# Performance work log

Hardware: AMD Instinct MI355X
Metric: run time of the kernel (lower is better)

## Reference

```python
import jax, jax.numpy as jnp
import numpy as np

N = 100000
E = 1600000
D_IN = 50
D_H = 128
D_OUT = 128
EPS = 1e-5


def setup_inputs() -> dict:
    key = jax.random.key(0)
    ks = jax.random.split(key, 24)
    def w(k, shape, fan_in):
        return jax.random.normal(k, shape, jnp.float32) / np.sqrt(fan_in)
    inp = {
        'x': jax.random.normal(ks[0], (N, D_IN), jnp.float32),
        'edge_src': jax.random.randint(ks[1], (E,), 0, N, jnp.int32),
        'edge_dst': jax.random.randint(ks[2], (E,), 0, N, jnp.int32),
        # SAGEConv 1: D_IN -> D_H
        'Wl1': w(ks[3], (D_IN, D_H), D_IN), 'Wr1': w(ks[4], (D_IN, D_H), D_IN), 'b1': jnp.zeros((D_H,), jnp.float32),
        # SAGEConv 2: D_H -> D_H
        'Wl2': w(ks[5], (D_H, D_H), D_H), 'Wr2': w(ks[6], (D_H, D_H), D_H), 'b2': jnp.zeros((D_H,), jnp.float32),
        # SAGEConv 3: D_H -> D_OUT
        'Wl3': w(ks[7], (D_H, D_OUT), D_H), 'Wr3': w(ks[8], (D_H, D_OUT), D_H), 'b3': jnp.zeros((D_OUT,), jnp.float32),
        # skip linears (no bias)
        'Ws1': w(ks[9], (D_IN, D_H), D_IN), 'Ws2': w(ks[10], (D_IN, D_H), D_IN),
        # LayerNorm affine
        'lnw1': jnp.ones((D_H,), jnp.float32), 'lnb1': jnp.zeros((D_H,), jnp.float32),
        'lnw2': jnp.ones((D_H,), jnp.float32), 'lnb2': jnp.zeros((D_H,), jnp.float32),
        'lnw3': jnp.ones((D_OUT,), jnp.float32), 'lnb3': jnp.zeros((D_OUT,), jnp.float32),
        # PReLU scalar slopes (PyG init 0.25)
        'a1': jnp.float32(0.25), 'a2': jnp.float32(0.25), 'a3': jnp.float32(0.25),
    }
    return inp


def _sage(x, src, dst, Wl, Wr, b):
    # mean aggregation of source features at destinations, then linear + root
    msg = x[src]                                              # [E, d]
    agg = jax.ops.segment_sum(msg, dst, num_segments=N)       # [N, d]
    cnt = jax.ops.segment_sum(jnp.ones((src.shape[0],), x.dtype), dst, num_segments=N)
    mean = agg / jnp.maximum(cnt, 1.0)[:, None]
    return mean @ Wl + x @ Wr + b


def _graph_ln(x, w, b):
    # PyG LayerNorm mode='graph', batch=None: normalize over all nodes+channels
    xc = x - jnp.mean(x)
    std = jnp.sqrt(jnp.mean(xc * xc))
    return (xc / (std + EPS)) * w + b


def _prelu(x, a):
    return jnp.where(x >= 0, x, a * x)


def reference(x, edge_src, edge_dst, Wl1, Wr1, b1, Wl2, Wr2, b2, Wl3, Wr3, b3,
              Ws1, Ws2, lnw1, lnb1, lnw2, lnb2, lnw3, lnb3, a1, a2, a3):
    h1 = _sage(x, edge_src, edge_dst, Wl1, Wr1, b1)
    h1 = _prelu(_graph_ln(h1, lnw1, lnb1), a1)
    h2 = _sage(h1 + x @ Ws1, edge_src, edge_dst, Wl2, Wr2, b2)
    h2 = _prelu(_graph_ln(h2, lnw2, lnb2), a2)
    ret = _sage(h1 + h2 + x @ Ws2, edge_src, edge_dst, Wl3, Wr3, b3)
    ret = _prelu(_graph_ln(ret, lnw3, lnb3), a3)
    return ret
```

## Files before the change

kernel.cpp:

```cpp
#include <hip/hip_runtime.h>

#define D_IN 50
#define LN_EPS 1e-5f
#define BSH 8
#define MAXB 512

typedef __bf16 bf16_t;
typedef bf16_t bf16x8 __attribute__((ext_vector_type(8)));
typedef bf16_t bf16x4 __attribute__((ext_vector_type(4)));
typedef float f32x4_t __attribute__((ext_vector_type(4)));
typedef float f32x2_t __attribute__((ext_vector_type(2)));

#define ACCP(r, A)                                                            \
    {                                                                         \
        A[0] += (f32x2_t){__uint_as_float((r).x << 16),                       \
                          __uint_as_float((r).x & 0xffff0000u)};              \
        A[1] += (f32x2_t){__uint_as_float((r).y << 16),                       \
                          __uint_as_float((r).y & 0xffff0000u)};              \
        A[2] += (f32x2_t){__uint_as_float((r).z << 16),                       \
                          __uint_as_float((r).z & 0xffff0000u)};              \
        A[3] += (f32x2_t){__uint_as_float((r).w << 16),                       \
                          __uint_as_float((r).w & 0xffff0000u)};              \
    }

__global__ void bucket_hist_k(const int* __restrict__ dst, int* __restrict__ bcnt,
                              double* __restrict__ lnacc, int e, int nb) {
    __shared__ int lh[MAXB];
    int t = threadIdx.x;
    if (blockIdx.x == 0 && t < 6) lnacc[t] = 0.0;
    for (int i = t; i < nb; i += 256) lh[i] = 0;
    __syncthreads();
    for (int i = blockIdx.x * 256 + t; i < e; i += gridDim.x * 256)
        atomicAdd(&lh[dst[i] >> BSH], 1);
    __syncthreads();
    for (int i = t; i < nb; i += 256) {
        int c = lh[i];
        if (c) atomicAdd(&bcnt[i * 16], c);
    }
}

__global__ void bscan_k(const int* __restrict__ bcnt, int* __restrict__ boff,
                        int* __restrict__ bpos, int nb, int e) {
    __shared__ int l[MAXB];
    int t = threadIdx.x;
    l[t] = (t < nb) ? bcnt[t * 16] : 0;
    __syncthreads();
    for (int off = 1; off < MAXB; off <<= 1) {
        int v = (t >= off) ? l[t - off] : 0;
        __syncthreads();
        l[t] += v;
        __syncthreads();
    }
    int excl = (t > 0) ? l[t - 1] : 0;
    if (t < nb) { boff[t] = excl; bpos[t * 16] = excl; }
    if (t == 0) boff[nb] = e;
}

__global__ void scatter_k(const int* __restrict__ src, const int* __restrict__ dst,
                          int* __restrict__ bpos, unsigned* __restrict__ pool,
                          int e, int nb) {
    __shared__ int lh[MAXB];
    __shared__ int lcur[MAXB];
    int t = threadIdx.x;
    for (int i = t; i < nb; i += 256) lh[i] = 0;
    __syncthreads();
    int chunk = (e + gridDim.x - 1) / gridDim.x;
    int s = blockIdx.x * chunk;
    int en = min(e, s + chunk);
    for (int i = s + t; i < en; i += 256)
        atomicAdd(&lh[dst[i] >> BSH], 1);
    __syncthreads();
    for (int i = t; i < nb; i += 256) {
        int c = lh[i];
        lcur[i] = c ? atomicAdd(&bpos[i * 16], c) : 0;
    }
    __syncthreads();
    for (int i = s + t; i < en; i += 256) {
        int d = dst[i];
        int p = atomicAdd(&lcur[d >> BSH], 1);
        pool[p] = (unsigned)src[i] | ((unsigned)(d & 255) << 17);
    }
}

__global__ void nhist_cfill_k(const unsigned* __restrict__ pool, const int* __restrict__ boff,
                              int* __restrict__ rp, int* __restrict__ col, int n) {
    __shared__ int lc[256];
    __shared__ int ls[256];
    __shared__ int lpos[256];
    int b = blockIdx.x, t = threadIdx.x;
    lc[t] = 0;
    __syncthreads();
    int s = boff[b], e = boff[b + 1];
    for (int i = s + t; i < e; i += 256) atomicAdd(&lc[pool[i] >> 17], 1);
    __syncthreads();
    int v = lc[t];
    ls[t] = v;
    __syncthreads();
    for (int off = 1; off < 256; off <<= 1) {
        int x = (t >= off) ? ls[t - off] : 0;
        __syncthreads();
        ls[t] += x;
        __syncthreads();
    }
    int excl = ls[t] - v;
    int nd = (b << BSH) + t;
    if (nd < n) rp[nd] = s + excl;
    if (nd == n - 1) rp[n] = e;
    lpos[t] = s + excl;
    __syncthreads();
    for (int i = s + t; i < e; i += 256) {
        unsigned pk = pool[i];
        int slot = atomicAdd(&lpos[pk >> 17], 1);
        col[slot] = (int)(pk & 0x1FFFFu);
    }
}

struct ConvDesc { const float* w; bf16_t* o; int kin; int kpad; };
struct ConvArgs { ConvDesc d[8]; };

__global__ void conv_w_k(ConvArgs args) {
    ConvDesc d = args.d[blockIdx.y];
    int i = blockIdx.x * 256 + threadIdx.x;
    int tot = 128 * d.kpad;
    if (i >= tot) return;
    int n = i / d.kpad, k = i - n * d.kpad;
    float v = (k < d.kin) ? d.w[(size_t)k * 128 + n] : 0.f;
    d.o[i] = (bf16_t)v;
}

__global__ void conv_x_k(const float* __restrict__ x, bf16_t* __restrict__ xb, int n) {
    int i = blockIdx.x * 256 + threadIdx.x;
    if (i >= n * 64) return;
    int node = i >> 6, k = i & 63;
    xb[i] = (k < D_IN) ? (bf16_t)x[node * D_IN + k] : (bf16_t)0.f;
}

__global__ void agg_bf64_k(const bf16_t* __restrict__ feat, const int* __restrict__ rp,
                           const int* __restrict__ col, bf16_t* __restrict__ mean, int n) {
    int wid = (blockIdx.x * blockDim.x + threadIdx.x) >> 6;
    int lane = threadIdx.x & 63;
    if (wid >= n) return;
    int start = rp[wid], end = rp[wid + 1];
    int lc = lane & 7;
    int g = lane >> 3;
    f32x2_t accA[4], accB[4];
#pragma unroll
    for (int k = 0; k < 4; k++) { accA[k] = (f32x2_t){0.f, 0.f}; accB[k] = (f32x2_t){0.f, 0.f}; }
    int e = start + g;
    if (e + 8 < end) {
        int i0 = col[e], i1 = col[e + 8];
        for (; e + 24 < end; e += 16) {
            uint4 r0 = *(const uint4*)(feat + (size_t)i0 * 64 + lc * 8);
            uint4 r1 = *(const uint4*)(feat + (size_t)i1 * 64 + lc * 8);
            i0 = col[e + 16];
            i1 = col[e + 24];
            ACCP(r0, accA);
            ACCP(r1, accB);
        }
        uint4 r0 = *(const uint4*)(feat + (size_t)i0 * 64 + lc * 8);
        uint4 r1 = *(const uint4*)(feat + (size_t)i1 * 64 + lc * 8);
        ACCP(r0, accA);
        ACCP(r1, accB);
        e += 16;
    }
    for (; e < end; e += 8) {
        uint4 r0 = *(const uint4*)(feat + (size_t)col[e] * 64 + lc * 8);
        ACCP(r0, accA);
    }
#pragma unroll
    for (int k = 0; k < 4; k++) accA[k] += accB[k];
    float aL[4], aH[4];
#pragma unroll
    for (int k = 0; k < 4; k++) { aL[k] = accA[k].x; aH[k] = accA[k].y; }
#pragma unroll
    for (int off = 8; off < 64; off <<= 1) {
#pragma unroll
        for (int k = 0; k < 4; k++) {
            aL[k] += __shfl_xor(aL[k], off);
            aH[k] += __shfl_xor(aH[k], off);
        }
    }
    int c = end - start;
    float invc = 1.f / (float)(c > 0 ? c : 1);
    if (lane < 8) {
        bf16x8 o;
#pragma unroll
        for (int k = 0; k < 4; k++) {
            o[2 * k] = (bf16_t)(aL[k] * invc);
            o[2 * k + 1] = (bf16_t)(aH[k] * invc);
        }
        *(bf16x8*)(mean + (size_t)wid * 64 + lc * 8) = o;
    }
}

__global__ void agg_bf128_k(const bf16_t* __restrict__ feat, const int* __restrict__ rp,
                            const int* __restrict__ col, bf16_t* __restrict__ mean, int n) {
    int wid = (blockIdx.x * blockDim.x + threadIdx.x) >> 6;
    int lane = threadIdx.x & 63;
    if (wid >= n) return;
    int start = rp[wid], end = rp[wid + 1];
    int lc = lane & 15;
    int g = lane >> 4;
    f32x2_t accA[4], accB[4];
#pragma unroll
    for (int k = 0; k < 4; k++) { accA[k] = (f32x2_t){0.f, 0.f}; accB[k] = (f32x2_t){0.f, 0.f}; }
    int e = start + g;
    if (e + 4 < end) {
        int i0 = col[e], i1 = col[e + 4];
        for (; e + 12 < end; e += 8) {
            uint4 r0 = *(const uint4*)(feat + (size_t)i0 * 128 + lc * 8);
            uint4 r1 = *(const uint4*)(feat + (size_t)i1 * 128 + lc * 8);
            i0 = col[e + 8];
            i1 = col[e + 12];
            ACCP(r0, accA);
            ACCP(r1, accB);
        }
        uint4 r0 = *(const uint4*)(feat + (size_t)i0 * 128 + lc * 8);
        uint4 r1 = *(const uint4*)(feat + (size_t)i1 * 128 + lc * 8);
        ACCP(r0, accA);
        ACCP(r1, accB);
        e += 8;
    }
    for (; e < end; e += 4) {
        uint4 r0 = *(const uint4*)(feat + (size_t)col[e] * 128 + lc * 8);
        ACCP(r0, accA);
    }
#pragma unroll
    for (int k = 0; k < 4; k++) accA[k] += accB[k];
    float aL[4], aH[4];
#pragma unroll
    for (int k = 0; k < 4; k++) { aL[k] = accA[k].x; aH[k] = accA[k].y; }
#pragma unroll
    for (int off = 16; off < 64; off <<= 1) {
#pragma unroll
        for (int k = 0; k < 4; k++) {
            aL[k] += __shfl_xor(aL[k], off);
            aH[k] += __shfl_xor(aH[k], off);
        }
    }
    int c = end - start;
    float invc = 1.f / (float)(c > 0 ? c : 1);
    if (lane < 16) {
        bf16x8 o;
#pragma unroll
        for (int k = 0; k < 4; k++) {
            o[2 * k] = (bf16_t)(aL[k] * invc);
            o[2 * k + 1] = (bf16_t)(aH[k] * invc);
        }
        *(bf16x8*)(mean + (size_t)wid * 128 + lc * 8) = o;
    }
}

template <int KPAD, bool DUAL>
__global__ __launch_bounds__(256) void mfma_gemm_k(
    const bf16_t* __restrict__ A, const bf16_t* __restrict__ B,
    const bf16_t* __restrict__ WlT, const bf16_t* __restrict__ WrT,
    const float* __restrict__ bias,
    bf16_t* __restrict__ out, double* __restrict__ lnacc, int M) {
    constexpr int KC = KPAD / 32;
    constexpr int WELE = 8 * KC * 64 * 8;
    __shared__ bf16_t lwl[WELE];
    __shared__ bf16_t lwr[DUAL ? WELE : 8];
    __shared__ float rsum[4], rsum2[4];

    const int tid = threadIdx.x;
    for (int ch = tid; ch < 8 * KC * 64; ch += 256) {
        int nt = ch / (KC * 64);
        int rem = ch - nt * (KC * 64);
        int c = rem >> 6;
        int ln = rem & 63;
        int m = ln & 15, q = ln >> 4;
        size_t srcoff = (size_t)(nt * 16 + m) * KPAD + c * 32 + q * 8;
        *(bf16x8*)&lwl[ch * 8] = *(const bf16x8*)(WlT + srcoff);
        if (DUAL) *(bf16x8*)&lwr[ch * 8] = *(const bf16x8*)(WrT + srcoff);
    }
    __syncthreads();

    const int w = tid >> 6;
    const int wid = blockIdx.x * 4 + w;
    const int lane = tid & 63;
    const int row0 = wid * 32;
    const int m = lane & 15;
    const int q = lane >> 4;
    const bool act = row0 < M;

    float lsum = 0.f, lsum2 = 0.f;
    if (act) {
        bf16x8 af[2][KC], bfr[DUAL ? 2 : 1][DUAL ? KC : 1];
#pragma unroll
        for (int s = 0; s < 2; s++) {
            const bf16_t* ar = A + (size_t)(row0 + s * 16 + m) * KPAD + q * 8;
#pragma unroll
            for (int c = 0; c < KC; c++) af[s][c] = *(const bf16x8*)(ar + c * 32);
            if (DUAL) {
                const bf16_t* br = B + (size_t)(row0 + s * 16 + m) * KPAD + q * 8;
#pragma unroll
                for (int c = 0; c < KC; c++) bfr[s][c] = *(const bf16x8*)(br + c * 32);
            }
        }
#pragma unroll
        for (int nt = 0; nt < 8; nt++) {
            f32x4_t acc0 = {0.f, 0.f, 0.f, 0.f};
            f32x4_t acc1 = {0.f, 0.f, 0.f, 0.f};
#pragma unroll
            for (int c = 0; c < KC; c++) {
                bf16x8 wv = *(const bf16x8*)&lwl[((nt * KC + c) * 64 + lane) * 8];
                acc0 = __builtin_amdgcn_mfma_f32_16x16x32_bf16(af[0][c], wv, acc0, 0, 0, 0);
                acc1 = __builtin_amdgcn_mfma_f32_16x16x32_bf16(af[1][c], wv, acc1, 0, 0, 0);
            }
            if (DUAL) {
#pragma unroll
                for (int c = 0; c < KC; c++) {
                    bf16x8 wv = *(const bf16x8*)&lwr[((nt * KC + c) * 64 + lane) * 8];
                    acc0 = __builtin_amdgcn_mfma_f32_16x16x32_bf16(bfr[0][c], wv, acc0, 0, 0, 0);
                    acc1 = __builtin_amdgcn_mfma_f32_16x16x32_bf16(bfr[1][c], wv, acc1, 0, 0, 0);
                }
            }
            float bv = bias ? bias[nt * 16 + m] : 0.f;
#pragma unroll
            for (int s = 0; s < 2; s++) {
                f32x4_t* ap = (s == 0) ? &acc0 : &acc1;
#pragma unroll
                for (int r = 0; r < 4; r++) {
                    int row = row0 + s * 16 + q * 4 + r;
                    if (row < M) {
                        float o = (*ap)[r] + bv;
                        out[(size_t)row * 128 + nt * 16 + m] = (bf16_t)o;
                        lsum += o; lsum2 += o * o;
                    }
                }
            }
        }
    }
    for (int off = 32; off > 0; off >>= 1) {
        lsum += __shfl_down(lsum, off);
        lsum2 += __shfl_down(lsum2, off);
    }
    if (lane == 0) { rsum[w] = lsum; rsum2[w] = lsum2; }
    __syncthreads();
    if (tid == 0) {
        double s = (double)rsum[0] + (double)rsum[1] + (double)rsum[2] + (double)rsum[3];
        double s2 = (double)rsum2[0] + (double)rsum2[1] + (double)rsum2[2] + (double)rsum2[3];
        unsafeAtomicAdd(&lnacc[0], s);
        unsafeAtomicAdd(&lnacc[1], s2);
    }
}

__global__ __launch_bounds__(256) void mfma_gemm3_k(
    const bf16_t* __restrict__ A, const bf16_t* __restrict__ B,
    const bf16_t* __restrict__ WlT, const bf16_t* __restrict__ WrT,
    const bf16_t* __restrict__ Ws1T, const bf16_t* __restrict__ Ws2T,
    const float* __restrict__ bias,
    bf16_t* __restrict__ outP, bf16_t* __restrict__ outC1, bf16_t* __restrict__ outC2,
    double* __restrict__ lnacc, int M) {
    constexpr int KC = 2;
    constexpr int WELE = 8 * KC * 64 * 8;
    __shared__ bf16_t lwl[WELE];
    __shared__ bf16_t lwr[WELE];
    __shared__ bf16_t ls1[WELE];
    __shared__ bf16_t ls2[WELE];
    __shared__ float rsum[4], rsum2[4];

    const int tid = threadIdx.x;
    for (int ch = tid; ch < 8 * KC * 64; ch += 256) {
        int nt = ch / (KC * 64);
        int rem = ch - nt * (KC * 64);
        int c = rem >> 6;
        int ln = rem & 63;
        int m = ln & 15, q = ln >> 4;
        size_t srcoff = (size_t)(nt * 16 + m) * 64 + c * 32 + q * 8;
        *(bf16x8*)&lwl[ch * 8] = *(const bf16x8*)(WlT + srcoff);
        *(bf16x8*)&lwr[ch * 8] = *(const bf16x8*)(WrT + srcoff);
        *(bf16x8*)&ls1[ch * 8] = *(const bf16x8*)(Ws1T + srcoff);
        *(bf16x8*)&ls2[ch * 8] = *(const bf16x8*)(Ws2T + srcoff);
    }
    __syncthreads();

    const int w = tid >> 6;
    const int wid = blockIdx.x * 4 + w;
    const int lane = tid & 63;
    const int row0 = wid * 32;
    const int m = lane & 15;
    const int q = lane >> 4;
    const bool act = row0 < M;

    float lsum = 0.f, lsum2 = 0.f;
    if (act) {
        bf16x8 af[2][KC], bfr[2][KC];
#pragma unroll
        for (int s = 0; s < 2; s++) {
            const bf16_t* ar = A + (size_t)(row0 + s * 16 + m) * 64 + q * 8;
            const bf16_t* br = B + (size_t)(row0 + s * 16 + m) * 64 + q * 8;
#pragma unroll
            for (int c = 0; c < KC; c++) {
                af[s][c] = *(const bf16x8*)(ar + c * 32);
                bfr[s][c] = *(const bf16x8*)(br + c * 32);
            }
        }
#pragma unroll
        for (int nt = 0; nt < 8; nt++) {
            f32x4_t aP0 = {0.f, 0.f, 0.f, 0.f}, aP1 = {0.f, 0.f, 0.f, 0.f};
            f32x4_t a10 = {0.f, 0.f, 0.f, 0.f}, a11 = {0.f, 0.f, 0.f, 0.f};
            f32x4_t a20 = {0.f, 0.f, 0.f, 0.f}, a21 = {0.f, 0.f, 0.f, 0.f};
#pragma unroll
            for (int c = 0; c < KC; c++) {
                int wi = ((nt * KC + c) * 64 + lane) * 8;
                bf16x8 wl = *(const bf16x8*)&lwl[wi];
                bf16x8 wr = *(const bf16x8*)&lwr[wi];
                bf16x8 w1 = *(const bf16x8*)&ls1[wi];
                bf16x8 w2 = *(const bf16x8*)&ls2[wi];
                aP0 = __builtin_amdgcn_mfma_f32_16x16x32_bf16(af[0][c], wl, aP0, 0, 0, 0);
                aP1 = __builtin_amdgcn_mfma_f32_16x16x32_bf16(af[1][c], wl, aP1, 0, 0, 0);
                aP0 = __builtin_amdgcn_mfma_f32_16x16x32_bf16(bfr[0][c], wr, aP0, 0, 0, 0);
                aP1 = __builtin_amdgcn_mfma_f32_16x16x32_bf16(bfr[1][c], wr, aP1, 0, 0, 0);
                a10 = __builtin_amdgcn_mfma_f32_16x16x32_bf16(bfr[0][c], w1, a10, 0, 0, 0);
                a11 = __builtin_amdgcn_mfma_f32_16x16x32_bf16(bfr[1][c], w1, a11, 0, 0, 0);
                a20 = __builtin_amdgcn_mfma_f32_16x16x32_bf16(bfr[0][c], w2, a20, 0, 0, 0);
                a21 = __builtin_amdgcn_mfma_f32_16x16x32_bf16(bfr[1][c], w2, a21, 0, 0, 0);
            }
            float bv = bias[nt * 16 + m];
#pragma unroll
            for (int s = 0; s < 2; s++) {
                f32x4_t* pP = (s == 0) ? &aP0 : &aP1;
                f32x4_t* p1 = (s == 0) ? &a10 : &a11;
                f32x4_t* p2 = (s == 0) ? &a20 : &a21;
#pragma unroll
                for (int r = 0; r < 4; r++) {
                    int row = row0 + s * 16 + q * 4 + r;
                    if (row < M) {
                        float o = (*pP)[r] + bv;
                        size_t oi = (size_t)row * 128 + nt * 16 + m;
                        outP[oi] = (bf16_t)o;
                        outC1[oi] = (bf16_t)(*p1)[r];
                        outC2[oi] = (bf16_t)(*p2)[r];
                        lsum += o; lsum2 += o * o;
                    }
                }
            }
        }
    }
    for (int off = 32; off > 0; off >>= 1) {
        lsum += __shfl_down(lsum, off);
        lsum2 += __shfl_down(lsum2, off);
    }
    if (lane == 0) { rsum[w] = lsum; rsum2[w] = lsum2; }
    __syncthreads();
    if (tid == 0) {
        double s = (double)rsum[0] + (double)rsum[1] + (double)rsum[2] + (double)rsum[3];
        double s2 = (double)rsum2[0] + (double)rsum2[1] + (double)rsum2[2] + (double)rsum2[3];
        unsafeAtomicAdd(&lnacc[0], s);
        unsafeAtomicAdd(&lnacc[1], s2);
    }
}

template <int MODE>
__global__ void ln_prelu_k(const bf16_t* __restrict__ pre, const bf16_t* __restrict__ h1in,
                           const bf16_t* __restrict__ s,
                           const float* __restrict__ lnw, const float* __restrict__ lnb,
                           const float* __restrict__ a_ptr, const double* __restrict__ acc,
                           void* __restrict__ out0v, void* __restrict__ out1v, int total) {
    int i = blockIdx.x * blockDim.x + threadIdx.x;
    if (i * 8 >= total) return;
    double cinv = 1.0 / (double)total;
    double mm = acc[0] * cinv;
    double var = acc[1] * cinv - mm * mm;
    float stdv = (float)sqrt(var > 0.0 ? var : 0.0);
    float scale = 1.0f / (stdv + LN_EPS);
    float mf = (float)mm;
    float a = a_ptr[0];
    int c8 = i & 15;
    float4 w0 = ((const float4*)lnw)[c8 * 2];
    float4 w1 = ((const float4*)lnw)[c8 * 2 + 1];
    float4 b0 = ((const float4*)lnb)[c8 * 2];
    float4 b1 = ((const float4*)lnb)[c8 * 2 + 1];
    float wv[8] = {w0.x, w0.y, w0.z, w0.w, w1.x, w1.y, w1.z, w1.w};
    float bv[8] = {b0.x, b0.y, b0.z, b0.w, b1.x, b1.y, b1.z, b1.w};
    bf16x8 p8 = ((const bf16x8*)pre)[i];
    float h[8];
#pragma unroll
    for (int k = 0; k < 8; k++) {
        float v = ((float)p8[k] - mf) * scale * wv[k] + bv[k];
        h[k] = v >= 0.f ? v : a * v;
    }
    if (MODE == 1) {
        bf16x8 hb, tb;
        bf16x8 sv = ((const bf16x8*)s)[i];
#pragma unroll
        for (int k = 0; k < 8; k++) {
            hb[k] = (bf16_t)h[k];
            tb[k] = (bf16_t)(h[k] + (float)sv[k]);
        }
        ((bf16x8*)out0v)[i] = hb;
        ((bf16x8*)out1v)[i] = tb;
    } else if (MODE == 2) {
        bf16x8 hv = ((const bf16x8*)h1in)[i];
        bf16x8 sv = ((const bf16x8*)s)[i];
        bf16x8 tb;
#pragma unroll
        for (int k = 0; k < 8; k++)
            tb[k] = (bf16_t)((float)hv[k] + h[k] + (float)sv[k]);
        ((bf16x8*)out0v)[i] = tb;
    } else {
        float4 o0 = {h[0], h[1], h[2], h[3]};
        float4 o1 = {h[4], h[5], h[6], h[7]};
        ((float4*)out0v)[i * 2] = o0;
        ((float4*)out0v)[i * 2 + 1] = o1;
    }
}

extern "C" void kernel_launch(void* const* d_in, const int* in_sizes, int n_in,
                              void* d_out, int out_size, void* d_ws, size_t ws_size,
                              hipStream_t stream) {
    const float* x    = (const float*)d_in[0];
    const int*   esrc = (const int*)d_in[1];
    const int*   edst = (const int*)d_in[2];
    const float* Wl1  = (const float*)d_in[3];
    const float* Wr1  = (const float*)d_in[4];
    const float* b1   = (const float*)d_in[5];
    const float* Wl2  = (const float*)d_in[6];
    const float* Wr2  = (const float*)d_in[7];
    const float* b2   = (const float*)d_in[8];
    const float* Wl3  = (const float*)d_in[9];
    const float* Wr3  = (const float*)d_in[10];
    const float* b3   = (const float*)d_in[11];
    const float* Ws1  = (const float*)d_in[12];
    const float* Ws2  = (const float*)d_in[13];
    const float* lnw1 = (const float*)d_in[14];
    const float* lnb1 = (const float*)d_in[15];
    const float* lnw2 = (const float*)d_in[16];
    const float* lnb2 = (const float*)d_in[17];
    const float* lnw3 = (const float*)d_in[18];
    const float* lnb3 = (const float*)d_in[19];
    const float* a1   = (const float*)d_in[20];
    const float* a2   = (const float*)d_in[21];
    const float* a3   = (const float*)d_in[22];

    const int N = in_sizes[0] / D_IN;
    const int E = in_sizes[1];
    const int NB = (N + 255) >> BSH;

    char* ws = (char*)d_ws;
    size_t off = 0;
    auto alloc = [&](size_t bytes) -> void* {
        void* p = ws + off;
        off += (bytes + 255) & ~(size_t)255;
        return p;
    };
    bf16_t* xb   = (bf16_t*)alloc((size_t)N * 64 * 2);
    bf16_t* mean = (bf16_t*)alloc((size_t)N * 128 * 2);
    bf16_t* PRE  = (bf16_t*)alloc((size_t)N * 128 * 2);
    bf16_t* C1   = (bf16_t*)alloc((size_t)N * 128 * 2);
    bf16_t* C2   = (bf16_t*)alloc((size_t)N * 128 * 2);
    bf16_t* h1b  = (bf16_t*)alloc((size_t)N * 128 * 2);
    bf16_t* TB   = (bf16_t*)alloc((size_t)N * 128 * 2);
    bf16_t* WT   = (bf16_t*)alloc((size_t)(4 * 128 * 64 + 4 * 128 * 128) * 2);
    int* rp   = (int*)alloc((size_t)(N + 1) * 4);
    int* col  = (int*)alloc((size_t)E * 4);
    int* bcnt = (int*)alloc((size_t)MAXB * 16 * 4);
    int* boff = (int*)alloc((size_t)(MAXB + 1) * 4);
    int* bpos = (int*)alloc((size_t)MAXB * 16 * 4);
    unsigned* pool = (unsigned*)alloc((size_t)E * 4);
    double* lnacc = (double*)alloc(6 * 8);

    bf16_t* Wl1T = WT;
    bf16_t* Wr1T = Wl1T + 128 * 64;
    bf16_t* Ws1T = Wr1T + 128 * 64;
    bf16_t* Ws2T = Ws1T + 128 * 64;
    bf16_t* Wl2T = Ws2T + 128 * 64;
    bf16_t* Wr2T = Wl2T + 128 * 128;
    bf16_t* Wl3T = Wr2T + 128 * 128;
    bf16_t* Wr3T = Wl3T + 128 * 128;

    hipMemsetAsync(bcnt, 0, (size_t)MAXB * 16 * 4, stream);

    bucket_hist_k<<<256, 256, 0, stream>>>(edst, bcnt, lnacc, E, NB);
    bscan_k<<<1, MAXB, 0, stream>>>(bcnt, boff, bpos, NB, E);
    scatter_k<<<256, 256, 0, stream>>>(esrc, edst, bpos, pool, E, NB);
    nhist_cfill_k<<<NB, 256, 0, stream>>>(pool, boff, rp, col, N);

    ConvArgs ca;
    ca.d[0] = {Wl1, Wl1T, 50, 64};
    ca.d[1] = {Wr1, Wr1T, 50, 64};
    ca.d[2] = {Ws1, Ws1T, 50, 64};
    ca.d[3] = {Ws2, Ws2T, 50, 64};
    ca.d[4] = {Wl2, Wl2T, 128, 128};
    ca.d[5] = {Wr2, Wr2T, 128, 128};
    ca.d[6] = {Wl3, Wl3T, 128, 128};
    ca.d[7] = {Wr3, Wr3T, 128, 128};
    conv_w_k<<<dim3(64, 8), 256, 0, stream>>>(ca);
    conv_x_k<<<(N * 64 + 255) / 256, 256, 0, stream>>>(x, xb, N);

    const int aggBlocks = ((N * 64) + 255) / 256;
    const int tiles = (N + 31) / 32;
    const int gemmBlocks = (tiles + 3) / 4;
    const int lnBlocks = (N * 128 / 8 + 255) / 256;
    const int total = N * 128;

    agg_bf64_k<<<aggBlocks, 256, 0, stream>>>(xb, rp, col, mean, N);
    mfma_gemm3_k<<<gemmBlocks, 256, 0, stream>>>(
        mean, xb, Wl1T, Wr1T, Ws1T, Ws2T, b1, PRE, C1, C2, lnacc + 0, N);
    ln_prelu_k<1><<<lnBlocks, 256, 0, stream>>>(
        PRE, nullptr, C1, lnw1, lnb1, a1, lnacc + 0, h1b, TB, total);

    agg_bf128_k<<<aggBlocks, 256, 0, stream>>>(TB, rp, col, mean, N);
    mfma_gemm_k<128, true><<<gemmBlocks, 256, 0, stream>>>(
        mean, TB, Wl2T, Wr2T, b2, PRE, lnacc + 2, N);
    ln_prelu_k<2><<<lnBlocks, 256, 0, stream>>>(
        PRE, h1b, C2, lnw2, lnb2, a2, lnacc + 2, TB, nullptr, total);

    agg_bf128_k<<<aggBlocks, 256, 0, stream>>>(TB, rp, col, mean, N);
    mfma_gemm_k<128, true><<<gemmBlocks, 256, 0, stream>>>(
        mean, TB, Wl3T, Wr3T, b3, PRE, lnacc + 4, N);
    ln_prelu_k<3><<<lnBlocks, 256, 0, stream>>>(
        PRE, nullptr, nullptr, lnw3, lnb3, a3, lnacc + 4, d_out, nullptr, total);
}
```

Baseline: 549.2 us.

## Stage GEMM outputs in LDS for coalesced 16-byte stores, read some weights from global

Both MFMA GEMM kernels now write each 16-row output tile into a padded per-wave LDS staging buffer, then store it to global memory as 16-byte vectors. This replaces the scattered 2-byte bf16 stores from the accumulator layout. The loops are reordered to handle one 16-row slice at a time. To free LDS for the staging buffer, the Wr weights (dual GEMM) and the Ws1/Ws2 skip weights are read straight from global memory or cache inside the inner loop, which may add load latency. There is no barrier between the LDS writes and reads of the per-wave buffer, so correctness relies on wave-level execution.

```diff
diff --git a/kernel.cpp b/kernel.cpp
--- a/kernel.cpp
+++ b/kernel.cpp
@@ -7,9 +7,10 @@
 
 typedef __bf16 bf16_t;
 typedef bf16_t bf16x8 __attribute__((ext_vector_type(8)));
-typedef bf16_t bf16x4 __attribute__((ext_vector_type(4)));
 typedef float f32x4_t __attribute__((ext_vector_type(4)));
 typedef float f32x2_t __attribute__((ext_vector_type(2)));
+
+#define STRIDE_ST 136
 
 #define ACCP(r, A)                                                            \
     {                                                                         \
@@ -260,7 +261,7 @@
     constexpr int KC = KPAD / 32;
     constexpr int WELE = 8 * KC * 64 * 8;
     __shared__ bf16_t lwl[WELE];
-    __shared__ bf16_t lwr[DUAL ? WELE : 8];
+    __shared__ __align__(16) bf16_t lst[4][16 * STRIDE_ST];
     __shared__ float rsum[4], rsum2[4];
 
     const int tid = threadIdx.x;
@@ -269,10 +270,9 @@
         int rem = ch - nt * (KC * 64);
         int c = rem >> 6;
         int ln = rem & 63;
-        int m = ln & 15, q = ln >> 4;
-        size_t srcoff = (size_t)(nt * 16 + m) * KPAD + c * 32 + q * 8;
+        int mm = ln & 15, qq = ln >> 4;
+        size_t srcoff = (size_t)(nt * 16 + mm) * KPAD + c * 32 + qq * 8;
         *(bf16x8*)&lwl[ch * 8] = *(const bf16x8*)(WlT + srcoff);
-        if (DUAL) *(bf16x8*)&lwr[ch * 8] = *(const bf16x8*)(WrT + srcoff);
     }
     __syncthreads();
 
@@ -298,37 +298,43 @@
                 for (int c = 0; c < KC; c++) bfr[s][c] = *(const bf16x8*)(br + c * 32);
             }
         }
-#pragma unroll
-        for (int nt = 0; nt < 8; nt++) {
-            f32x4_t acc0 = {0.f, 0.f, 0.f, 0.f};
-            f32x4_t acc1 = {0.f, 0.f, 0.f, 0.f};
-#pragma unroll
-            for (int c = 0; c < KC; c++) {
-                bf16x8 wv = *(const bf16x8*)&lwl[((nt * KC + c) * 64 + lane) * 8];
-                acc0 = __builtin_amdgcn_mfma_f32_16x16x32_bf16(af[0][c], wv, acc0, 0, 0, 0);
-                acc1 = __builtin_amdgcn_mfma_f32_16x16x32_bf16(af[1][c], wv, acc1, 0, 0, 0);
-            }
-            if (DUAL) {
+        bf16_t* st = lst[w];
+#pragma unroll
+        for (int s = 0; s < 2; s++) {
+#pragma unroll
+            for (int nt = 0; nt < 8; nt++) {
+                f32x4_t acc = {0.f, 0.f, 0.f, 0.f};
 #pragma unroll
                 for (int c = 0; c < KC; c++) {
-                    bf16x8 wv = *(const bf16x8*)&lwr[((nt * KC + c) * 64 + lane) * 8];
-                    acc0 = __builtin_amdgcn_mfma_f32_16x16x32_bf16(bfr[0][c], wv, acc0, 0, 0, 0);
-                    acc1 = __builtin_amdgcn_mfma_f32_16x16x32_bf16(bfr[1][c], wv, acc1, 0, 0, 0);
+                    bf16x8 wl = *(const bf16x8*)&lwl[((nt * KC + c) * 64 + lane) * 8];
+                    acc = __builtin_amdgcn_mfma_f32_16x16x32_bf16(af[s][c], wl, acc, 0, 0, 0);
+                }
+                if (DUAL) {
+#pragma unroll
+                    for (int c = 0; c < KC; c++) {
+                        size_t woff = (size_t)(nt * 16 + m) * KPAD + c * 32 + q * 8;
+                        bf16x8 wr = *(const bf16x8*)(WrT + woff);
+                        acc = __builtin_amdgcn_mfma_f32_16x16x32_bf16(bfr[s][c], wr, acc, 0, 0, 0);
+                    }
+                }
+                float bv = bias ? bias[nt * 16 + m] : 0.f;
+#pragma unroll
+                for (int r = 0; r < 4; r++) {
+                    float o = acc[r] + bv;
+                    int row = row0 + s * 16 + q * 4 + r;
+                    if (row < M) { lsum += o; lsum2 += o * o; }
+                    st[(q * 4 + r) * STRIDE_ST + nt * 16 + m] = (bf16_t)o;
                 }
             }
-            float bv = bias ? bias[nt * 16 + m] : 0.f;
-#pragma unroll
-            for (int s = 0; s < 2; s++) {
-                f32x4_t* ap = (s == 0) ? &acc0 : &acc1;
-#pragma unroll
-                for (int r = 0; r < 4; r++) {
-                    int row = row0 + s * 16 + q * 4 + r;
-                    if (row < M) {
-                        float o = (*ap)[r] + bv;
-                        out[(size_t)row * 128 + nt * 16 + m] = (bf16_t)o;
-                        lsum += o; lsum2 += o * o;
-                    }
-                }
+            int rowbase = row0 + s * 16;
+#pragma unroll
+            for (int k = 0; k < 4; k++) {
+                int chunk = k * 64 + lane;
+                int rr = chunk >> 4;
+                int co = (chunk & 15) * 8;
+                int row = rowbase + rr;
+                bf16x8 v = *(bf16x8*)&st[rr * STRIDE_ST + co];
+                if (row < M) *(bf16x8*)(out + (size_t)row * 128 + co) = v;
             }
         }
     }
@@ -357,8 +363,7 @@
     constexpr int WELE = 8 * KC * 64 * 8;
     __shared__ bf16_t lwl[WELE];
     __shared__ bf16_t lwr[WELE];
-    __shared__ bf16_t ls1[WELE];
-    __shared__ bf16_t ls2[WELE];
+    __shared__ __align__(16) bf16_t lst[4][16 * STRIDE_ST];
     __shared__ float rsum[4], rsum2[4];
 
     const int tid = threadIdx.x;
@@ -367,12 +372,10 @@
         int rem = ch - nt * (KC * 64);
         int c = rem >> 6;
         int ln = rem & 63;
-        int m = ln & 15, q = ln >> 4;
-        size_t srcoff = (size_t)(nt * 16 + m) * 64 + c * 32 + q * 8;
+        int mm = ln & 15, qq = ln >> 4;
+        size_t srcoff = (size_t)(nt * 16 + mm) * 64 + c * 32 + qq * 8;
         *(bf16x8*)&lwl[ch * 8] = *(const bf16x8*)(WlT + srcoff);
         *(bf16x8*)&lwr[ch * 8] = *(const bf16x8*)(WrT + srcoff);
-        *(bf16x8*)&ls1[ch * 8] = *(const bf16x8*)(Ws1T + srcoff);
-        *(bf16x8*)&ls2[ch * 8] = *(const bf16x8*)(Ws2T + srcoff);
     }
     __syncthreads();
 
@@ -397,44 +400,70 @@
                 bfr[s][c] = *(const bf16x8*)(br + c * 32);
             }
         }
-#pragma unroll
-        for (int nt = 0; nt < 8; nt++) {
-            f32x4_t aP0 = {0.f, 0.f, 0.f, 0.f}, aP1 = {0.f, 0.f, 0.f, 0.f};
-            f32x4_t a10 = {0.f, 0.f, 0.f, 0.f}, a11 = {0.f, 0.f, 0.f, 0.f};
-            f32x4_t a20 = {0.f, 0.f, 0.f, 0.f}, a21 = {0.f, 0.f, 0.f, 0.f};
-#pragma unroll
-            for (int c = 0; c < KC; c++) {
-                int wi = ((nt * KC + c) * 64 + lane) * 8;
-                bf16x8 wl = *(const bf16x8*)&lwl[wi];
-                bf16x8 wr = *(const bf16x8*)&lwr[wi];
-                bf16x8 w1 = *(const bf16x8*)&ls1[wi];
-                bf16x8 w2 = *(const bf16x8*)&ls2[wi];
-                aP0 = __builtin_amdgcn_mfma_f32_16x16x32_bf16(af[0][c], wl, aP0, 0, 0, 0);
-                aP1 = __builtin_amdgcn_mfma_f32_16x16x32_bf16(af[1][c], wl, aP1, 0, 0, 0);
-                aP0 = __builtin_amdgcn_mfma_f32_16x16x32_bf16(bfr[0][c], wr, aP0, 0, 0, 0);
-                aP1 = __builtin_amdgcn_mfma_f32_16x16x32_bf16(bfr[1][c], wr, aP1, 0, 0, 0);
-                a10 = __builtin_amdgcn_mfma_f32_16x16x32_bf16(bfr[0][c], w1, a10, 0, 0, 0);
-                a11 = __builtin_amdgcn_mfma_f32_16x16x32_bf16(bfr[1][c], w1, a11, 0, 0, 0);
-                a20 = __builtin_amdgcn_mfma_f32_16x16x32_bf16(bfr[0][c], w2, a20, 0, 0, 0);
-                a21 = __builtin_amdgcn_mfma_f32_16x16x32_bf16(bfr[1][c], w2, a21, 0, 0, 0);
+        bf16_t* st = lst[w];
+
+#pragma unroll
+        for (int s = 0; s < 2; s++) {
+#pragma unroll
+            for (int nt = 0; nt < 8; nt++) {
+                f32x4_t acc = {0.f, 0.f, 0.f, 0.f};
+#pragma unroll
+                for (int c = 0; c < KC; c++) {
+                    int wi = ((nt * KC + c) * 64 + lane) * 8;
+                    bf16x8 wl = *(const bf16x8*)&lwl[wi];
+                    bf16x8 wr = *(const bf16x8*)&lwr[wi];
+                    acc = __builtin_amdgcn_mfma_f32_16x16x32_bf16(af[s][c], wl, acc, 0, 0, 0);
+                    acc = __builtin_amdgcn_mfma_f32_16x16x32_bf16(bfr[s][c], wr, acc, 0, 0, 0);
+                }
+                float bv = bias[nt * 16 + m];
+#pragma unroll
+                for (int r = 0; r < 4; r++) {
+                    float o = acc[r] + bv;
+                    int row = row0 + s * 16 + q * 4 + r;
+                    if (row < M) { lsum += o; lsum2 += o * o; }
+                    st[(q * 4 + r) * STRIDE_ST + nt * 16 + m] = (bf16_t)o;
+                }
             }
-            float bv = bias[nt * 16 + m];
+            int rowbase = row0 + s * 16;
+#pragma unroll
+            for (int k = 0; k < 4; k++) {
+                int chunk = k * 64 + lane;
+                int rr = chunk >> 4;
+                int co = (chunk & 15) * 8;
+                int row = rowbase + rr;
+                bf16x8 v = *(bf16x8*)&st[rr * STRIDE_ST + co];
+                if (row < M) *(bf16x8*)(outP + (size_t)row * 128 + co) = v;
+            }
+        }
+
+#pragma unroll
+        for (int p = 0; p < 2; p++) {
+            const bf16_t* WT = (p == 0) ? Ws1T : Ws2T;
+            bf16_t* outC = (p == 0) ? outC1 : outC2;
 #pragma unroll
             for (int s = 0; s < 2; s++) {
-                f32x4_t* pP = (s == 0) ? &aP0 : &aP1;
-                f32x4_t* p1 = (s == 0) ? &a10 : &a11;
-                f32x4_t* p2 = (s == 0) ? &a20 : &a21;
-#pragma unroll
-                for (int r = 0; r < 4; r++) {
-                    int row = row0 + s * 16 + q * 4 + r;
-                    if (row < M) {
-                        float o = (*pP)[r] + bv;
-                        size_t oi = (size_t)row * 128 + nt * 16 + m;
-                        outP[oi] = (bf16_t)o;
-                        outC1[oi] = (bf16_t)(*p1)[r];
-                        outC2[oi] = (bf16_t)(*p2)[r];
-                        lsum += o; lsum2 += o * o;
+#pragma unroll
+                for (int nt = 0; nt < 8; nt++) {
+                    f32x4_t acc = {0.f, 0.f, 0.f, 0.f};
+#pragma unroll
+                    for (int c = 0; c < KC; c++) {
+                        size_t woff = (size_t)(nt * 16 + m) * 64 + c * 32 + q * 8;
+                        bf16x8 wv = *(const bf16x8*)(WT + woff);
+                        acc = __builtin_amdgcn_mfma_f32_16x16x32_bf16(bfr[s][c], wv, acc, 0, 0, 0);
                     }
+#pragma unroll
+                    for (int r = 0; r < 4; r++)
+                        st[(q * 4 + r) * STRIDE_ST + nt * 16 + m] = (bf16_t)acc[r];
+                }
+                int rowbase = row0 + s * 16;
+#pragma unroll
+                for (int k = 0; k < 4; k++) {
+                    int chunk = k * 64 + lane;
+                    int rr = chunk >> 4;
+                    int co = (chunk & 15) * 8;
+                    int row = rowbase + rr;
+                    bf16x8 v = *(bf16x8*)&st[rr * STRIDE_ST + co];
+                    if (row < M) *(bf16x8*)(outC + (size_t)row * 128 + co) = v;
                 }
             }
         }
```

Result: no change. 547.2 us (-0.4%).
